# Optimization experiments

Hardware: AMD Instinct MI355X
Metric: run time of the kernel (lower is better)

The kernel has to match this reference:

```python
import jax, jax.numpy as jnp
import numpy as np

B, N, M, H = 2, 2048, 1024, 16
DK = M // H

def setup_inputs() -> dict:
    key = jax.random.key(0)
    ks = jax.random.split(key, 10)
    s = 1.0 / np.sqrt(M)
    return {
        "x": jax.random.normal(ks[0], (B, N, M), jnp.float32),
        "mask": jax.random.uniform(ks[1], (B, 1, N, N), jnp.float32),
        "Wq": jax.random.normal(ks[2], (M, M), jnp.float32) * s,
        "bq": jax.random.normal(ks[3], (M,), jnp.float32) * 0.01,
        "Wk": jax.random.normal(ks[4], (M, M), jnp.float32) * s,
        "bk": jax.random.normal(ks[5], (M,), jnp.float32) * 0.01,
        "Wv": jax.random.normal(ks[6], (M, M), jnp.float32) * s,
        "bv": jax.random.normal(ks[7], (M,), jnp.float32) * 0.01,
        "Wo": jax.random.normal(ks[8], (M, M), jnp.float32) * s,
        "bo": jax.random.normal(ks[9], (M,), jnp.float32) * 0.01,
    }

def reference(x, mask, Wq, bq, Wk, bk, Wv, bv, Wo, bo):
    Bv, Nv, Mv = x.shape
    # linear projections, split into heads: [B, H, N, DK]
    def proj(W, b):
        return (x @ W.T + b).reshape(Bv, Nv, H, DK).transpose(0, 2, 1, 3)
    q = proj(Wq, bq)
    k = proj(Wk, bk)
    v = proj(Wv, bv)
    # scaled scores [B, H, N, N], multiplicative mask pre-softmax
    scores = jnp.einsum('bhqd,bhkd->bhqk', q, k) / jnp.sqrt(jnp.float32(DK))
    scores = scores * mask  # mask broadcasts over heads
    attn = jax.nn.softmax(scores, axis=-1)
    # dropout in eval/reference: identity
    out = jnp.einsum('bhqk,bhkd->bhqd', attn, v)  # [B, H, N, DK]
    concat = out.transpose(0, 2, 1, 3).reshape(Bv, Nv, Mv)
    return concat @ Wo.T + bo
```

## Files before the change

kernel.cpp:

```cpp
#include <hip/hip_runtime.h>
#include <hip/hip_bf16.h>
#include <math.h>


typedef __attribute__((ext_vector_type(8))) short bf16x8;
typedef __attribute__((ext_vector_type(4))) float f32x4;

typedef __attribute__((address_space(1))) void gvoid;
typedef __attribute__((address_space(3))) void lvoid;

__device__ __forceinline__ void gll16(const void* g, void* l) {
    __builtin_amdgcn_global_load_lds(
        (gvoid*)(unsigned long long)g,
        (lvoid*)(unsigned int)(unsigned long long)l,
        16, 0, 0);
}

__device__ __forceinline__ short f2b(float f) {
    union { __hip_bfloat16 h; short s; } u;
    u.h = __float2bfloat16(f);
    return u.s;
}
__device__ __forceinline__ float b2f(short s) {
    union { short s; __hip_bfloat16 h; } u;
    u.s = s;
    return __bfloat162float(u.h);
}

__device__ __forceinline__ int sw8(int r, int k8) {
    return (r << 6) + ((k8 ^ (r & 7)) << 3);
}
__device__ __forceinline__ int swe(int r, int k) {
    return (r << 6) + (((k >> 3) ^ (r & 7)) << 3) + (k & 7);
}

#define PLANE   4194304UL
#define OFF_WH  (0UL * PLANE)
#define OFF_XH  (1UL * PLANE)
#define OFF_QH  (2UL * PLANE)
#define OFF_QL  (3UL * PLANE)
#define OFF_KH  (4UL * PLANE)
#define OFF_VTH (5UL * PLANE)
#define OFF_CH  (6UL * PLANE)

#define QSCALE  (0.125f * 1.44269504f)

__global__ __launch_bounds__(256) void split_wx(
    const float* __restrict__ Wq, const float* __restrict__ Wk,
    const float* __restrict__ Wv, const float* __restrict__ Wo,
    const float* __restrict__ x,
    unsigned short* __restrict__ wh, unsigned short* __restrict__ xh)
{
    const int i = blockIdx.x * 256 + threadIdx.x;
    if (i < 1048576) {
        const float* src = (i < 262144) ? Wq : (i < 524288) ? Wk
                         : (i < 786432) ? Wv : Wo;
        const float sc = (i < 262144) ? QSCALE : 1.0f;
        const int local = i & 262143;
        float4 v = ((const float4*)src)[local];
        short4 h;
        h.x = f2b(v.x * sc); h.y = f2b(v.y * sc);
        h.z = f2b(v.z * sc); h.w = f2b(v.w * sc);
        ((short4*)(wh + (size_t)(i >> 18) * 1048576))[local] = h;
    } else {
        const int local = i - 1048576;
        float4 v = ((const float4*)x)[local];
        short4 h;
        h.x = f2b(v.x); h.y = f2b(v.y); h.z = f2b(v.z); h.w = f2b(v.w);
        ((short4*)xh)[local] = h;
    }
}

__global__ __launch_bounds__(256, 4) void gemm_qkv(
    unsigned short* __restrict__ wsS,
    const float* __restrict__ bq, const float* __restrict__ bk,
    const float* __restrict__ bv)
{
    __shared__ unsigned short Ash[128 * 64];
    __shared__ unsigned short Bsh[128 * 64];

    const int mode = blockIdx.z;
    const unsigned short* Ah = wsS + OFF_XH;
    const unsigned short* Wh = wsS + OFF_WH + (size_t)mode * 1048576;

    const int tid  = threadIdx.x;
    const int lane = tid & 63;
    const int lm   = lane & 15;
    const int quad = lane >> 4;
    const int w    = tid >> 6;
    const int wr   = w >> 1, wc = w & 1;

    const int row0 = blockIdx.y * 128;
    const int col0 = blockIdx.x * 128;

    const int srow = lane >> 3;
    const int soct = (lane & 7) ^ (srow & 7);

    f32x4 acc[4][4] = {};

    for (int k0 = 0; k0 < 1024; k0 += 64) {
        if (k0) __syncthreads();
        #pragma unroll
        for (int i = 0; i < 4; ++i) {
            const int rb = w * 32 + i * 8;
            gll16(&Ah[(size_t)(row0 + rb + srow) * 1024 + k0 + soct * 8],
                  &Ash[rb * 64]);
            gll16(&Wh[(size_t)(col0 + rb + srow) * 1024 + k0 + soct * 8],
                  &Bsh[rb * 64]);
        }
        __syncthreads();
        #pragma unroll
        for (int ks = 0; ks < 2; ++ks) {
            bf16x8 afh[4], bfh[4];
            #pragma unroll
            for (int mi = 0; mi < 4; ++mi)
                afh[mi] = *(const bf16x8*)&Ash[sw8(wr * 64 + mi * 16 + lm, ks * 4 + quad)];
            #pragma unroll
            for (int ni = 0; ni < 4; ++ni)
                bfh[ni] = *(const bf16x8*)&Bsh[sw8(wc * 64 + ni * 16 + lm, ks * 4 + quad)];
            #pragma unroll
            for (int mi = 0; mi < 4; ++mi) {
                #pragma unroll
                for (int ni = 0; ni < 4; ++ni)
                    acc[mi][ni] = __builtin_amdgcn_mfma_f32_16x16x32_bf16(
                        afh[mi], bfh[ni], acc[mi][ni], 0, 0, 0);
            }
        }
    }

    unsigned short* qh  = wsS + OFF_QH;
    unsigned short* ql  = wsS + OFF_QL;
    unsigned short* kh  = wsS + OFF_KH;
    unsigned short* vth = wsS + OFF_VTH;
    const float* bias = (mode == 0) ? bq : (mode == 1) ? bk : bv;
    const float bscale = (mode == 0) ? QSCALE : 1.0f;

    #pragma unroll
    for (int ni = 0; ni < 4; ++ni) {
        const int f = col0 + wc * 64 + ni * 16 + lm;
        const float bvv = bias[f] * bscale;
        const int h = f >> 6, d = f & 63;
        #pragma unroll
        for (int mi = 0; mi < 4; ++mi) {
            #pragma unroll
            for (int j = 0; j < 4; ++j) {
                const int row = row0 + wr * 64 + mi * 16 + quad * 4 + j;
                const float val = acc[mi][ni][j] + bvv;
                const int bb = row >> 11, n = row & 2047;
                const short hs = f2b(val);
                if (mode == 0) {
                    const size_t idx = ((size_t)(bb * 16 + h) * 2048 + n) * 64 + d;
                    qh[idx] = hs;
                    ql[idx] = f2b(val - b2f(hs));
                } else if (mode == 1) {
                    kh[((size_t)(bb * 16 + h) * 2048 + n) * 64 + d] = hs;
                } else {
                    vth[((size_t)(bb * 16 + h) * 64 + d) * 2048 + n] = hs;
                }
            }
        }
    }
}

__global__ __launch_bounds__(512, 2) void gemm_out(
    const unsigned short* __restrict__ Ah,
    unsigned short* __restrict__ wsS,
    const float* __restrict__ bias_p, float* __restrict__ oout)
{
    __shared__ unsigned short Ash[128 * 64];
    __shared__ unsigned short Bsh[128 * 64];

    const unsigned short* Wh = wsS + OFF_WH + 3UL * 1048576;

    const int tid  = threadIdx.x;
    const int lane = tid & 63;
    const int lm   = lane & 15;
    const int quad = lane >> 4;
    const int w    = tid >> 6;
    const int wr   = w >> 2;
    const int wc   = w & 3;

    const int row0 = blockIdx.y * 128;
    const int col0 = blockIdx.x * 128;

    const int srow = lane >> 3;
    const int soct = (lane & 7) ^ (srow & 7);

    f32x4 acc[4][2] = {};

    for (int k0 = 0; k0 < 1024; k0 += 64) {
        if (k0) __syncthreads();
        #pragma unroll
        for (int i = 0; i < 2; ++i) {
            const int rb = w * 16 + i * 8;
            gll16(&Ah[(size_t)(row0 + rb + srow) * 1024 + k0 + soct * 8],
                  &Ash[rb * 64]);
            gll16(&Wh[(size_t)(col0 + rb + srow) * 1024 + k0 + soct * 8],
                  &Bsh[rb * 64]);
        }
        __syncthreads();
        #pragma unroll
        for (int ks = 0; ks < 2; ++ks) {
            bf16x8 afh[4], bfh[2];
            #pragma unroll
            for (int mi = 0; mi < 4; ++mi)
                afh[mi] = *(const bf16x8*)&Ash[sw8(wr * 64 + mi * 16 + lm, ks * 4 + quad)];
            #pragma unroll
            for (int ni = 0; ni < 2; ++ni)
                bfh[ni] = *(const bf16x8*)&Bsh[sw8(wc * 32 + ni * 16 + lm, ks * 4 + quad)];
            #pragma unroll
            for (int mi = 0; mi < 4; ++mi) {
                #pragma unroll
                for (int ni = 0; ni < 2; ++ni)
                    acc[mi][ni] = __builtin_amdgcn_mfma_f32_16x16x32_bf16(
                        afh[mi], bfh[ni], acc[mi][ni], 0, 0, 0);
            }
        }
    }

    #pragma unroll
    for (int ni = 0; ni < 2; ++ni) {
        const int f = col0 + wc * 32 + ni * 16 + lm;
        const float bvv = bias_p[f];
        #pragma unroll
        for (int mi = 0; mi < 4; ++mi) {
            #pragma unroll
            for (int j = 0; j < 4; ++j) {
                const int row = row0 + wr * 64 + mi * 16 + quad * 4 + j;
                oout[(size_t)row * 1024 + f] = acc[mi][ni][j] + bvv;
            }
        }
    }
}

__global__ __launch_bounds__(512, 4) void attn_fast(
    const unsigned short* __restrict__ wsS, const float* __restrict__ mask,
    unsigned short* __restrict__ ch)
{
    __shared__ unsigned short Ksh[2][64 * 64];
    __shared__ unsigned short Vth[2][64 * 64];
    __shared__ unsigned short Psh[8][16 * 64];

    const int tid  = threadIdx.x;
    const int lane = tid & 63;
    const int lm   = lane & 15;
    const int quad = lane >> 4;
    const int w    = tid >> 6;

    const int q0 = blockIdx.x * 128;
    const int h  = blockIdx.y;
    const int b  = blockIdx.z;
    const int bh = b * 16 + h;

    const unsigned short* Qhg = wsS + OFF_QH  + (size_t)bh * 2048 * 64;
    const unsigned short* Qlg = wsS + OFF_QL  + (size_t)bh * 2048 * 64;
    const unsigned short* Khg = wsS + OFF_KH  + (size_t)bh * 2048 * 64;
    const unsigned short* Vhg = wsS + OFF_VTH + (size_t)bh * 64 * 2048;

    bf16x8 qfh[2], qfl[2];
    #pragma unroll
    for (int ks = 0; ks < 2; ++ks) {
        const size_t qo = (size_t)(q0 + w * 16 + lm) * 64 + ks * 32 + quad * 8;
        qfh[ks] = *(const bf16x8*)&Qhg[qo];
        qfl[ks] = *(const bf16x8*)&Qlg[qo];
    }

    const int srow = lane >> 3;
    const int soct = (lane & 7) ^ (srow & 7);
    const int rb   = w * 8;

    const int qwbase = q0 + w * 16 + quad * 4;
    const float* mp0 = mask + (size_t)b * 2048 * 2048
                     + (size_t)(qwbase + 0) * 2048 + lm;
    const float* mp1 = mp0 + 2048;
    const float* mp2 = mp0 + 4096;
    const float* mp3 = mp0 + 6144;

    gll16(&Khg[(size_t)(rb + srow) * 64 + soct * 8],   &Ksh[0][rb * 64]);
    gll16(&Vhg[(size_t)(rb + srow) * 2048 + soct * 8], &Vth[0][rb * 64]);

    f32x4 o[4] = {};
    float lsum[4] = {0.f, 0.f, 0.f, 0.f};

    for (int t = 0; t < 32; ++t) {
        const int k0 = t * 64;
        const int p  = t & 1;

        __syncthreads();

        float mr0[4], mr1[4], mr2[4], mr3[4];
        #pragma unroll
        for (int ni = 0; ni < 4; ++ni) {
            mr0[ni] = mp0[ni * 16];
            mr1[ni] = mp1[ni * 16];
            mr2[ni] = mp2[ni * 16];
            mr3[ni] = mp3[ni * 16];
        }
        mp0 += 64; mp1 += 64; mp2 += 64; mp3 += 64;

        if (t < 31) {
            gll16(&Khg[(size_t)(k0 + 64 + rb + srow) * 64 + soct * 8],
                  &Ksh[1 - p][rb * 64]);
            gll16(&Vhg[(size_t)(rb + srow) * 2048 + k0 + 64 + soct * 8],
                  &Vth[1 - p][rb * 64]);
        }

        f32x4 s[4] = {};
        #pragma unroll
        for (int ks = 0; ks < 2; ++ks) {
            #pragma unroll
            for (int ni = 0; ni < 4; ++ni) {
                bf16x8 kh = *(const bf16x8*)&Ksh[p][sw8(ni * 16 + lm, ks * 4 + quad)];
                s[ni] = __builtin_amdgcn_mfma_f32_16x16x32_bf16(qfh[ks], kh, s[ni], 0, 0, 0);
                s[ni] = __builtin_amdgcn_mfma_f32_16x16x32_bf16(qfl[ks], kh, s[ni], 0, 0, 0);
            }
        }

        #pragma unroll
        for (int ni = 0; ni < 4; ++ni) {
            const float pv0 = __builtin_amdgcn_exp2f(s[ni][0] * mr0[ni]);
            const float pv1 = __builtin_amdgcn_exp2f(s[ni][1] * mr1[ni]);
            const float pv2 = __builtin_amdgcn_exp2f(s[ni][2] * mr2[ni]);
            const float pv3 = __builtin_amdgcn_exp2f(s[ni][3] * mr3[ni]);
            lsum[0] += pv0; lsum[1] += pv1; lsum[2] += pv2; lsum[3] += pv3;
            Psh[w][swe(quad * 4 + 0, ni * 16 + lm)] = f2b(pv0);
            Psh[w][swe(quad * 4 + 1, ni * 16 + lm)] = f2b(pv1);
            Psh[w][swe(quad * 4 + 2, ni * 16 + lm)] = f2b(pv2);
            Psh[w][swe(quad * 4 + 3, ni * 16 + lm)] = f2b(pv3);
        }

        #pragma unroll
        for (int ks = 0; ks < 2; ++ks) {
            bf16x8 ph = *(const bf16x8*)&Psh[w][sw8(lm, ks * 4 + quad)];
            #pragma unroll
            for (int ni = 0; ni < 4; ++ni) {
                bf16x8 vh = *(const bf16x8*)&Vth[p][sw8(ni * 16 + lm, ks * 4 + quad)];
                o[ni] = __builtin_amdgcn_mfma_f32_16x16x32_bf16(ph, vh, o[ni], 0, 0, 0);
            }
        }
    }

    #pragma unroll
    for (int j = 0; j < 4; ++j) {
        float ls = lsum[j];
        ls += __shfl_xor(ls, 1);
        ls += __shfl_xor(ls, 2);
        ls += __shfl_xor(ls, 4);
        ls += __shfl_xor(ls, 8);
        const float inv = 1.0f / ls;
        const int q = qwbase + j;
        #pragma unroll
        for (int ni = 0; ni < 4; ++ni)
            ch[((size_t)b * 2048 + q) * 1024 + h * 64 + ni * 16 + lm] =
                (unsigned short)f2b(o[ni][j] * inv);
    }
}

extern "C" void kernel_launch(void* const* d_in, const int* in_sizes, int n_in,
                              void* d_out, int out_size, void* d_ws, size_t ws_size,
                              hipStream_t stream) {
    const float* x    = (const float*)d_in[0];
    const float* mask = (const float*)d_in[1];
    const float* Wq   = (const float*)d_in[2];
    const float* bq   = (const float*)d_in[3];
    const float* Wk   = (const float*)d_in[4];
    const float* bk   = (const float*)d_in[5];
    const float* Wv   = (const float*)d_in[6];
    const float* bv   = (const float*)d_in[7];
    const float* Wo   = (const float*)d_in[8];
    const float* bo   = (const float*)d_in[9];

    unsigned short* wsS = (unsigned short*)d_ws;

    split_wx<<<8192, 256, 0, stream>>>(Wq, Wk, Wv, Wo, x,
        wsS + OFF_WH, wsS + OFF_XH);

    gemm_qkv<<<dim3(8, 32, 3), 256, 0, stream>>>(wsS, bq, bk, bv);

    attn_fast<<<dim3(16, 16, 2), 512, 0, stream>>>(wsS, mask, wsS + OFF_CH);

    gemm_out<<<dim3(8, 32), 512, 0, stream>>>(
        wsS + OFF_CH, wsS, bo, (float*)d_out);
}
```

Baseline: 249.5 us.

## Software-pipeline QK^T one tile ahead of softmax and PV in attention loop

Restructures the attention loop so the QK^T MFMAs for tile t+1 are issued between the exp/P-store and the PV MFMAs of tile t, with K prefetched two tiles ahead and mask values loaded one tile ahead. It also raises wave priority around the MFMA blocks with s_setprio. The goal is to hide exp and LDS latency behind matrix work and overlap global loads for longer. The cost is higher register pressure from holding two score tiles and two mask sets, which may lower occupancy, plus a more complex buffer-reuse schedule.

```diff
diff --git a/kernel.cpp b/kernel.cpp
--- a/kernel.cpp
+++ b/kernel.cpp
@@ -276,52 +276,63 @@
     const float* mp2 = mp0 + 4096;
     const float* mp3 = mp0 + 6144;
 
-    gll16(&Khg[(size_t)(rb + srow) * 64 + soct * 8],   &Ksh[0][rb * 64]);
-    gll16(&Vhg[(size_t)(rb + srow) * 2048 + soct * 8], &Vth[0][rb * 64]);
+    gll16(&Khg[(size_t)(rb + srow) * 64 + soct * 8],        &Ksh[0][rb * 64]);
+    gll16(&Vhg[(size_t)(rb + srow) * 2048 + soct * 8],      &Vth[0][rb * 64]);
+    gll16(&Khg[(size_t)(64 + rb + srow) * 64 + soct * 8],   &Ksh[1][rb * 64]);
+
+    float mc0[4], mc1[4], mc2[4], mc3[4];
+    #pragma unroll
+    for (int ni = 0; ni < 4; ++ni) {
+        mc0[ni] = mp0[ni * 16];
+        mc1[ni] = mp1[ni * 16];
+        mc2[ni] = mp2[ni * 16];
+        mc3[ni] = mp3[ni * 16];
+    }
+    mp0 += 64; mp1 += 64; mp2 += 64; mp3 += 64;
+
+    __syncthreads();
+
+    f32x4 scur[4] = {};
+    __builtin_amdgcn_s_setprio(1);
+    #pragma unroll
+    for (int ks = 0; ks < 2; ++ks) {
+        #pragma unroll
+        for (int ni = 0; ni < 4; ++ni) {
+            bf16x8 kh = *(const bf16x8*)&Ksh[0][sw8(ni * 16 + lm, ks * 4 + quad)];
+            scur[ni] = __builtin_amdgcn_mfma_f32_16x16x32_bf16(qfh[ks], kh, scur[ni], 0, 0, 0);
+            scur[ni] = __builtin_amdgcn_mfma_f32_16x16x32_bf16(qfl[ks], kh, scur[ni], 0, 0, 0);
+        }
+    }
+    __builtin_amdgcn_s_setprio(0);
 
     f32x4 o[4] = {};
     float lsum[4] = {0.f, 0.f, 0.f, 0.f};
 
     for (int t = 0; t < 32; ++t) {
-        const int k0 = t * 64;
-        const int p  = t & 1;
+        const int p = t & 1;
 
         __syncthreads();
 
-        float mr0[4], mr1[4], mr2[4], mr3[4];
+        float mn0[4], mn1[4], mn2[4], mn3[4];
+        if (t < 31) {
+            #pragma unroll
+            for (int ni = 0; ni < 4; ++ni) {
+                mn0[ni] = mp0[ni * 16];
+                mn1[ni] = mp1[ni * 16];
+                mn2[ni] = mp2[ni * 16];
+                mn3[ni] = mp3[ni * 16];
+            }
+            mp0 += 64; mp1 += 64; mp2 += 64; mp3 += 64;
+            gll16(&Vhg[(size_t)(rb + srow) * 2048 + (t + 1) * 64 + soct * 8],
+                  &Vth[1 - p][rb * 64]);
+        }
+
         #pragma unroll
         for (int ni = 0; ni < 4; ++ni) {
-            mr0[ni] = mp0[ni * 16];
-            mr1[ni] = mp1[ni * 16];
-            mr2[ni] = mp2[ni * 16];
-            mr3[ni] = mp3[ni * 16];
-        }
-        mp0 += 64; mp1 += 64; mp2 += 64; mp3 += 64;
-
-        if (t < 31) {
-            gll16(&Khg[(size_t)(k0 + 64 + rb + srow) * 64 + soct * 8],
-                  &Ksh[1 - p][rb * 64]);
-            gll16(&Vhg[(size_t)(rb + srow) * 2048 + k0 + 64 + soct * 8],
-                  &Vth[1 - p][rb * 64]);
-        }
-
-        f32x4 s[4] = {};
-        #pragma unroll
-        for (int ks = 0; ks < 2; ++ks) {
-            #pragma unroll
-            for (int ni = 0; ni < 4; ++ni) {
-                bf16x8 kh = *(const bf16x8*)&Ksh[p][sw8(ni * 16 + lm, ks * 4 + quad)];
-                s[ni] = __builtin_amdgcn_mfma_f32_16x16x32_bf16(qfh[ks], kh, s[ni], 0, 0, 0);
-                s[ni] = __builtin_amdgcn_mfma_f32_16x16x32_bf16(qfl[ks], kh, s[ni], 0, 0, 0);
-            }
-        }
-
-        #pragma unroll
-        for (int ni = 0; ni < 4; ++ni) {
-            const float pv0 = __builtin_amdgcn_exp2f(s[ni][0] * mr0[ni]);
-            const float pv1 = __builtin_amdgcn_exp2f(s[ni][1] * mr1[ni]);
-            const float pv2 = __builtin_amdgcn_exp2f(s[ni][2] * mr2[ni]);
-            const float pv3 = __builtin_amdgcn_exp2f(s[ni][3] * mr3[ni]);
+            const float pv0 = __builtin_amdgcn_exp2f(scur[ni][0] * mc0[ni]);
+            const float pv1 = __builtin_amdgcn_exp2f(scur[ni][1] * mc1[ni]);
+            const float pv2 = __builtin_amdgcn_exp2f(scur[ni][2] * mc2[ni]);
+            const float pv3 = __builtin_amdgcn_exp2f(scur[ni][3] * mc3[ni]);
             lsum[0] += pv0; lsum[1] += pv1; lsum[2] += pv2; lsum[3] += pv3;
             Psh[w][swe(quad * 4 + 0, ni * 16 + lm)] = f2b(pv0);
             Psh[w][swe(quad * 4 + 1, ni * 16 + lm)] = f2b(pv1);
@@ -329,6 +340,26 @@
             Psh[w][swe(quad * 4 + 3, ni * 16 + lm)] = f2b(pv3);
         }
 
+        if (t < 30)
+            gll16(&Khg[(size_t)((t + 2) * 64 + rb + srow) * 64 + soct * 8],
+                  &Ksh[p][rb * 64]);
+
+        f32x4 snew[4] = {};
+        if (t < 31) {
+            __builtin_amdgcn_s_setprio(1);
+            #pragma unroll
+            for (int ks = 0; ks < 2; ++ks) {
+                #pragma unroll
+                for (int ni = 0; ni < 4; ++ni) {
+                    bf16x8 kh = *(const bf16x8*)&Ksh[1 - p][sw8(ni * 16 + lm, ks * 4 + quad)];
+                    snew[ni] = __builtin_amdgcn_mfma_f32_16x16x32_bf16(qfh[ks], kh, snew[ni], 0, 0, 0);
+                    snew[ni] = __builtin_amdgcn_mfma_f32_16x16x32_bf16(qfl[ks], kh, snew[ni], 0, 0, 0);
+                }
+            }
+            __builtin_amdgcn_s_setprio(0);
+        }
+
+        __builtin_amdgcn_s_setprio(1);
         #pragma unroll
         for (int ks = 0; ks < 2; ++ks) {
             bf16x8 ph = *(const bf16x8*)&Psh[w][sw8(lm, ks * 4 + quad)];
@@ -336,6 +367,16 @@
             for (int ni = 0; ni < 4; ++ni) {
                 bf16x8 vh = *(const bf16x8*)&Vth[p][sw8(ni * 16 + lm, ks * 4 + quad)];
                 o[ni] = __builtin_amdgcn_mfma_f32_16x16x32_bf16(ph, vh, o[ni], 0, 0, 0);
+            }
+        }
+        __builtin_amdgcn_s_setprio(0);
+
+        if (t < 31) {
+            #pragma unroll
+            for (int ni = 0; ni < 4; ++ni) {
+                scur[ni] = snew[ni];
+                mc0[ni] = mn0[ni]; mc1[ni] = mn1[ni];
+                mc2[ni] = mn2[ni]; mc3[ni] = mn3[ni];
             }
         }
     }
```

Result: faster. 236.9 us (-5.1%).
